# Kernel tuning notes

Measured on AMD Instinct MI355X. Metric: run time of the kernel, lower is better.

The kernel has to match this reference:

```python
import jax, jax.numpy as jnp
import numpy as np

QMIN, QMAX = 0.0, 255.0  # uint8 activation quantization range


def _qlinear(x, w_q, b, s_in, zp_in, s_w):
    """zentorch_qlinear: quantize fp32 x to uint8, int8 weight, dequant output.

    x:   [M, K] fp32
    w_q: [N, K] int8 values (stored int32), symmetric (weight zp = 0)
    b:   [N] fp32
    s_in, zp_in: scalars (activation scale / zero point)
    s_w: [N] per-output-channel weight scales
    """
    zp = zp_in.astype(jnp.float32)
    q = jnp.clip(jnp.round(x / s_in) + zp, QMIN, QMAX)      # fake-quant uint8
    x_dq = (q - zp) * s_in                                   # dequantized activation
    w_dq = w_q.astype(jnp.float32) * s_w[:, None]            # [N, K] dequant weight
    return x_dq @ w_dq.T + b                                 # [M, N] fp32


def setup_inputs() -> dict:
    key = jax.random.key(0)
    k1, k2, k3, k4 = jax.random.split(key, 4)
    M, K, N = 8192, 4096, 4096
    inp = {
        "input": jax.random.normal(k1, (M, K), dtype=jnp.float32),
        "weights": jax.random.randint(k2, (N, K), -128, 128, dtype=jnp.int32),
        "biases": jax.random.normal(k3, (N,), dtype=jnp.float32) * 0.1,
        "input_scales": jnp.array([0.05], dtype=jnp.float32),
        "input_zero_points": jnp.array([128], dtype=jnp.int32),
        "weight_scales": jax.random.uniform(k4, (N,), dtype=jnp.float32, minval=0.001, maxval=0.01),
        "weight_zero_points": jnp.zeros((N,), dtype=jnp.int32),
        "output_dtype": 0,  # 0 -> float32
    }
    return inp


def reference(input, weights, biases, input_scales, input_zero_points,
              weight_scales, weight_zero_points, output_dtype):
    s_in = input_scales[0]
    zp_in = input_zero_points[0]
    x = _qlinear(input, weights, biases, s_in, zp_in, weight_scales)
    x = _qlinear(x, weights, biases, s_in, zp_in, weight_scales)
    x = _qlinear(x, weights, biases, s_in, zp_in, weight_scales)
    return x
```

## Files before the change

kernel.cpp:

```cpp
#include <hip/hip_runtime.h>
#include <stdint.h>

#define M_DIM 8192
#define K_DIM 4096
#define N_DIM 4096
#define KTILES (K_DIM / 64)

typedef __attribute__((ext_vector_type(4))) int i32x4;

__global__ void pack_w_kernel(const int* __restrict__ w, char* __restrict__ wp,
                              int* __restrict__ corr, const int* __restrict__ zpp) {
  __shared__ int red[256];
  const int n = blockIdx.x;
  const int t = threadIdx.x;
  const int4* row = (const int4*)(w + (size_t)n * K_DIM);
  int s = 0;
  int words[4];
#pragma unroll
  for (int u = 0; u < 4; ++u) {
    int4 v = row[t * 4 + u];
    s += v.x + v.y + v.z + v.w;
    words[u] = (v.x & 255) | ((v.y & 255) << 8) | ((v.z & 255) << 16) | (v.w << 24);
  }
  ((int4*)(wp + (size_t)n * K_DIM))[t] = make_int4(words[0], words[1], words[2], words[3]);
  red[t] = s;
  __syncthreads();
  for (int off = 128; off > 0; off >>= 1) {
    if (t < off) red[t] += red[t + off];
    __syncthreads();
  }
  if (t == 0) corr[n] = (128 - zpp[0]) * red[0];
}

__global__ void quant_in_kernel(const float* __restrict__ x, char* __restrict__ q,
                                const float* __restrict__ sp, const int* __restrict__ zpp) {
  const int i = blockIdx.x * blockDim.x + threadIdx.x;
  const float s = sp[0];
  const float zp = (float)zpp[0];
  float4 v = ((const float4*)x)[i];
  float t0 = fminf(fmaxf(rintf(v.x / s) + zp, 0.f), 255.f);
  float t1 = fminf(fmaxf(rintf(v.y / s) + zp, 0.f), 255.f);
  float t2 = fminf(fmaxf(rintf(v.z / s) + zp, 0.f), 255.f);
  float t3 = fminf(fmaxf(rintf(v.w / s) + zp, 0.f), 255.f);
  int b0 = (int)t0 - 128, b1 = (int)t1 - 128, b2 = (int)t2 - 128, b3 = (int)t3 - 128;
  ((int*)q)[i] = (b0 & 255) | ((b1 & 255) << 8) | ((b2 & 255) << 16) | (b3 << 24);
}

#define STAGE16(SRC, DST)                                                     \
  __builtin_amdgcn_global_load_lds(                                           \
      (const __attribute__((address_space(1))) void*)(SRC),                   \
      (__attribute__((address_space(3))) void*)(DST), 16, 0, 0)

#define RD(p) (*(const i32x4*)(p))

#define TILE(SLOT, KSTG, DO_NEXT)                                             \
  {                                                                           \
    const char* bufA_ = &lds[SLOT][0][0];                                     \
    char* nA_ = &lds[((SLOT) + 3) & 3][0][0];                                 \
    char* nB_ = &lds[((SLOT) + 3) & 3][1][0];                                 \
    i32x4 a1_[4];                                                             \
    _Pragma("unroll") for (int i_ = 0; i_ < 4; ++i_)                          \
        a1_[i_] = RD(bufA_ + aoff[4 + i_]);                                   \
    STAGE16(asrc0 + (size_t)(KSTG) * 64, nA_ + o0_);                          \
    STAGE16(asrc1 + (size_t)(KSTG) * 64, nA_ + o1_);                          \
    __builtin_amdgcn_s_setprio(1);                                            \
    _Pragma("unroll") for (int i_ = 0; i_ < 4; ++i_)                          \
        _Pragma("unroll") for (int j_ = 0; j_ < 4; ++j_)                      \
            acc[i_][j_] = __builtin_amdgcn_mfma_i32_16x16x64_i8(              \
                a0[i_], b0[j_], acc[i_][j_], 0, 0, 0);                        \
    __builtin_amdgcn_s_setprio(0);                                            \
    i32x4 ta_[4], tb_[4];                                                     \
    if (DO_NEXT) {                                                            \
      const char* xA_ = &lds[((SLOT) + 1) & 3][0][0];                         \
      const char* xB_ = &lds[((SLOT) + 1) & 3][1][0];                         \
      _Pragma("unroll") for (int i_ = 0; i_ < 4; ++i_)                        \
          ta_[i_] = RD(xA_ + aoff[i_]);                                       \
      _Pragma("unroll") for (int j_ = 0; j_ < 4; ++j_)                        \
          tb_[j_] = RD(xB_ + boff[j_]);                                       \
    }                                                                         \
    STAGE16(bsrc0 + (size_t)(KSTG) * 64, nB_ + o0_);                          \
    STAGE16(bsrc1 + (size_t)(KSTG) * 64, nB_ + o1_);                          \
    __builtin_amdgcn_s_setprio(1);                                            \
    _Pragma("unroll") for (int i_ = 0; i_ < 4; ++i_)                          \
        _Pragma("unroll") for (int j_ = 0; j_ < 4; ++j_)                      \
            acc[4 + i_][j_] = __builtin_amdgcn_mfma_i32_16x16x64_i8(          \
                a1_[i_], b0[j_], acc[4 + i_][j_], 0, 0, 0);                   \
    __builtin_amdgcn_s_setprio(0);                                            \
    asm volatile("s_waitcnt vmcnt(4)" ::: "memory");                          \
    __builtin_amdgcn_s_barrier();                                             \
    if (DO_NEXT) {                                                            \
      _Pragma("unroll") for (int i_ = 0; i_ < 4; ++i_) a0[i_] = ta_[i_];      \
      _Pragma("unroll") for (int j_ = 0; j_ < 4; ++j_) b0[j_] = tb_[j_];      \
    }                                                                         \
  }

template <int WRITE_Q>
__global__ __launch_bounds__(512, 2) void gemm_kernel(
    const char* __restrict__ qa, const char* __restrict__ wb,
    const int* __restrict__ corr, const float* __restrict__ swp,
    const float* __restrict__ bias, const float* __restrict__ sp,
    const int* __restrict__ zpp, char* __restrict__ outq, float* __restrict__ outf) {
  __shared__ __align__(16) char lds[4][2][16384];
  const int tid = threadIdx.x;
  const int lane = tid & 63;
  const int w = tid >> 6;
  const int wr = w >> 2;
  const int wc = w & 3;
  const int bid = blockIdx.x;
  const int bm = bid & 31;
  const int bn = bid >> 5;
  const char* abase = qa + (size_t)bm * 256 * K_DIM;
  const char* bbase = wb + (size_t)bn * 256 * K_DIM;

  const int o0_ = tid * 16;
  const int o1_ = 8192 + tid * 16;
  const int r0_ = o0_ >> 6, r1_ = o1_ >> 6;
  const int g0_ = ((o0_ >> 4) & 3) ^ ((r0_ >> 1) & 3);
  const int g1_ = ((o1_ >> 4) & 3) ^ ((r1_ >> 1) & 3);
  const char* asrc0 = abase + (size_t)r0_ * K_DIM + g0_ * 16;
  const char* asrc1 = abase + (size_t)r1_ * K_DIM + g1_ * 16;
  const char* bsrc0 = bbase + (size_t)r0_ * K_DIM + g0_ * 16;
  const char* bsrc1 = bbase + (size_t)r1_ * K_DIM + g1_ * 16;

  const int rr = lane & 15;
  const int g = lane >> 4;
  int aoff[8], boff[4];
#pragma unroll
  for (int i = 0; i < 8; ++i) {
    const int row = wr * 128 + i * 16 + rr;
    aoff[i] = (row << 6) + ((g ^ ((row >> 1) & 3)) << 4);
  }
#pragma unroll
  for (int j = 0; j < 4; ++j) {
    const int row = wc * 64 + j * 16 + rr;
    boff[j] = (row << 6) + ((g ^ ((row >> 1) & 3)) << 4);
  }

  i32x4 acc[8][4] = {};

  STAGE16(asrc0, &lds[0][0][o0_]); STAGE16(asrc1, &lds[0][0][o1_]);
  STAGE16(bsrc0, &lds[0][1][o0_]); STAGE16(bsrc1, &lds[0][1][o1_]);
  STAGE16(asrc0 + 64, &lds[1][0][o0_]); STAGE16(asrc1 + 64, &lds[1][0][o1_]);
  STAGE16(bsrc0 + 64, &lds[1][1][o0_]); STAGE16(bsrc1 + 64, &lds[1][1][o1_]);
  STAGE16(asrc0 + 128, &lds[2][0][o0_]); STAGE16(asrc1 + 128, &lds[2][0][o1_]);
  STAGE16(bsrc0 + 128, &lds[2][1][o0_]); STAGE16(bsrc1 + 128, &lds[2][1][o1_]);
  asm volatile("s_waitcnt vmcnt(4)" ::: "memory");
  __builtin_amdgcn_s_barrier();

  i32x4 a0[4], b0[4];
#pragma unroll
  for (int i = 0; i < 4; ++i) a0[i] = RD(&lds[0][0][0] + aoff[i]);
#pragma unroll
  for (int j = 0; j < 4; ++j) b0[j] = RD(&lds[0][1][0] + boff[j]);

  for (int tb = 0; tb < (KTILES - 4) / 4; ++tb) {
    const int t0 = tb * 4;
#pragma unroll
    for (int u = 0; u < 4; ++u) {
      TILE(u, t0 + u + 3, 1);
    }
  }
  TILE(0, KTILES - 1, 1);
  TILE(1, KTILES - 1, 1);
  TILE(2, KTILES - 1, 1);
  TILE(3, KTILES - 1, 0);
  asm volatile("s_waitcnt vmcnt(0)" ::: "memory");

  const float s = sp[0];
  const float zpf = (float)zpp[0];
  const int m0 = bm * 256 + wr * 128 + (lane >> 4) * 4;
  const int n0 = bn * 256 + wc * 64 + (lane & 15);
#pragma unroll
  for (int j = 0; j < 4; ++j) {
    const int n = n0 + j * 16;
    const int cr = corr[n];
    const float fs = s * swp[n];
    const float bb = bias[n];
#pragma unroll
    for (int i = 0; i < 8; ++i) {
#pragma unroll
      for (int q = 0; q < 4; ++q) {
        const int m = m0 + i * 16 + q;
        float val = fs * (float)(acc[i][j][q] + cr) + bb;
        if (WRITE_Q) {
          float tq = fminf(fmaxf(rintf(val / s) + zpf, 0.f), 255.f);
          outq[(size_t)m * N_DIM + n] = (char)((int)tq - 128);
        } else {
          outf[(size_t)m * N_DIM + n] = val;
        }
      }
    }
  }
}

extern "C" void kernel_launch(void* const* d_in, const int* in_sizes, int n_in,
                              void* d_out, int out_size, void* d_ws, size_t ws_size,
                              hipStream_t stream) {
  const float* x = (const float*)d_in[0];
  const int* wq = (const int*)d_in[1];
  const float* bias = (const float*)d_in[2];
  const float* s_in = (const float*)d_in[3];
  const int* zp_in = (const int*)d_in[4];
  const float* s_w = (const float*)d_in[5];
  float* out = (float*)d_out;

  const size_t WP_BYTES = (size_t)N_DIM * K_DIM;
  const size_t Q_BYTES = (size_t)M_DIM * K_DIM;
  char* ws = (char*)d_ws;
  char* wp = ws;
  char* q1 = ws + WP_BYTES;
  char* q2 = q1 + Q_BYTES;
  int* corr = (int*)(q2 + Q_BYTES);
  const size_t NEEDED = WP_BYTES + 2 * Q_BYTES + (size_t)N_DIM * sizeof(int);
  if (ws_size < NEEDED) return;

  pack_w_kernel<<<N_DIM, 256, 0, stream>>>(wq, wp, corr, zp_in);
  quant_in_kernel<<<(M_DIM * K_DIM / 4) / 256, 256, 0, stream>>>(x, q1, s_in, zp_in);

  dim3 grid((M_DIM / 256) * (N_DIM / 256));
  dim3 blk(512);
  gemm_kernel<1><<<grid, blk, 0, stream>>>(q1, wp, corr, s_w, bias, s_in, zp_in, q2, nullptr);
  gemm_kernel<1><<<grid, blk, 0, stream>>>(q2, wp, corr, s_w, bias, s_in, zp_in, q1, nullptr);
  gemm_kernel<0><<<grid, blk, 0, stream>>>(q1, wp, corr, s_w, bias, s_in, zp_in, nullptr, out);
}
```

Before: 451.7 us.

## Restructure GEMM main loop into four barrier-interleaved MFMA phases with vectorized epilogue

```diff
diff --git a/kernel.cpp b/kernel.cpp
--- a/kernel.cpp
+++ b/kernel.cpp
@@ -53,45 +53,56 @@
 
 #define RD(p) (*(const i32x4*)(p))
 
-#define TILE(SLOT, KSTG, DO_NEXT)                                             \
+#define BAR __builtin_amdgcn_s_barrier()
+#define LGKM0 asm volatile("s_waitcnt lgkmcnt(0)" ::: "memory")
+#define SCHED0 __builtin_amdgcn_sched_barrier(0)
+
+#define MF8(I0, AV, J0, BV)                                                   \
+  _Pragma("unroll") for (int i_ = 0; i_ < 4; ++i_)                            \
+      _Pragma("unroll") for (int j_ = 0; j_ < 2; ++j_)                        \
+          acc[(I0) + i_][(J0) + j_] = __builtin_amdgcn_mfma_i32_16x16x64_i8(  \
+              AV[i_], BV[j_], acc[(I0) + i_][(J0) + j_], 0, 0, 0);
+
+#define TILE8(SLOT, KSTG)                                                     \
   {                                                                           \
-    const char* bufA_ = &lds[SLOT][0][0];                                     \
+    const char* sA_ = &lds[SLOT][0][0];                                       \
+    const char* sB_ = &lds[SLOT][1][0];                                       \
     char* nA_ = &lds[((SLOT) + 3) & 3][0][0];                                 \
     char* nB_ = &lds[((SLOT) + 3) & 3][1][0];                                 \
-    i32x4 a1_[4];                                                             \
+    i32x4 aL[4], aH[4], bL[2], bH[2];                                         \
+                                             \
     _Pragma("unroll") for (int i_ = 0; i_ < 4; ++i_)                          \
-        a1_[i_] = RD(bufA_ + aoff[4 + i_]);                                   \
-    STAGE16(asrc0 + (size_t)(KSTG) * 64, nA_ + o0_);                          \
-    STAGE16(asrc1 + (size_t)(KSTG) * 64, nA_ + o1_);                          \
-    __builtin_amdgcn_s_setprio(1);                                            \
+        aL[i_] = RD(sA_ + aoff[i_]);                                          \
+    bL[0] = RD(sB_ + boff[0]);                                                \
+    bL[1] = RD(sB_ + boff[1]);                                                \
+    STAGE16(asrc0 + (size_t)(KSTG), nA_ + o0_);                               \
+    BAR; LGKM0; SCHED0;                                                       \
+    __builtin_amdgcn_s_setprio(1); MF8(0, aL, 0, bL)                          \
+    __builtin_amdgcn_s_setprio(0);                                            \
+    BAR;                                                                      \
+                                             \
+    bH[0] = RD(sB_ + boff[2]);                                                \
+    bH[1] = RD(sB_ + boff[3]);                                                \
+    STAGE16(asrc1 + (size_t)(KSTG), nA_ + o1_);                               \
+    BAR; LGKM0; SCHED0;                                                       \
+    __builtin_amdgcn_s_setprio(1); MF8(0, aL, 2, bH)                          \
+    __builtin_amdgcn_s_setprio(0);                                            \
+    BAR;                                                                      \
+                                             \
     _Pragma("unroll") for (int i_ = 0; i_ < 4; ++i_)                          \
-        _Pragma("unroll") for (int j_ = 0; j_ < 4; ++j_)                      \
-            acc[i_][j_] = __builtin_amdgcn_mfma_i32_16x16x64_i8(              \
-                a0[i_], b0[j_], acc[i_][j_], 0, 0, 0);                        \
-    __builtin_amdgcn_s_setprio(0);                                            \
-    i32x4 ta_[4], tb_[4];                                                     \
-    if (DO_NEXT) {                                                            \
-      const char* xA_ = &lds[((SLOT) + 1) & 3][0][0];                         \
-      const char* xB_ = &lds[((SLOT) + 1) & 3][1][0];                         \
-      _Pragma("unroll") for (int i_ = 0; i_ < 4; ++i_)                        \
-          ta_[i_] = RD(xA_ + aoff[i_]);                                       \
-      _Pragma("unroll") for (int j_ = 0; j_ < 4; ++j_)                        \
-          tb_[j_] = RD(xB_ + boff[j_]);                                       \
-    }                                                                         \
-    STAGE16(bsrc0 + (size_t)(KSTG) * 64, nB_ + o0_);                          \
-    STAGE16(bsrc1 + (size_t)(KSTG) * 64, nB_ + o1_);                          \
-    __builtin_amdgcn_s_setprio(1);                                            \
-    _Pragma("unroll") for (int i_ = 0; i_ < 4; ++i_)                          \
-        _Pragma("unroll") for (int j_ = 0; j_ < 4; ++j_)                      \
-            acc[4 + i_][j_] = __builtin_amdgcn_mfma_i32_16x16x64_i8(          \
-                a1_[i_], b0[j_], acc[4 + i_][j_], 0, 0, 0);                   \
-    __builtin_amdgcn_s_setprio(0);                                            \
-    asm volatile("s_waitcnt vmcnt(4)" ::: "memory");                          \
-    __builtin_amdgcn_s_barrier();                                             \
-    if (DO_NEXT) {                                                            \
-      _Pragma("unroll") for (int i_ = 0; i_ < 4; ++i_) a0[i_] = ta_[i_];      \
-      _Pragma("unroll") for (int j_ = 0; j_ < 4; ++j_) b0[j_] = tb_[j_];      \
-    }                                                                         \
+        aH[i_] = RD(sA_ + aoff[4 + i_]);                                      \
+    STAGE16(bsrc0 + (size_t)(KSTG), nB_ + o0_);                               \
+    BAR; LGKM0; SCHED0;                                                       \
+    __builtin_amdgcn_s_setprio(1); MF8(4, aH, 2, bH)                          \
+    __builtin_amdgcn_s_setprio(0);                                            \
+    BAR;                                                                      \
+                                  \
+    STAGE16(bsrc1 + (size_t)(KSTG), nB_ + o1_);                               \
+    BAR; SCHED0;                                                              \
+    __builtin_amdgcn_s_setprio(1); MF8(4, aH, 0, bL)                          \
+    __builtin_amdgcn_s_setprio(0);                                            \
+    asm volatile("s_waitcnt vmcnt(8)" ::: "memory");                          \
+    BAR;                                                                      \
   }
 
 template <int WRITE_Q>
@@ -119,8 +130,10 @@
   const int g1_ = ((o1_ >> 4) & 3) ^ ((r1_ >> 1) & 3);
   const char* asrc0 = abase + (size_t)r0_ * K_DIM + g0_ * 16;
   const char* asrc1 = abase + (size_t)r1_ * K_DIM + g1_ * 16;
-  const char* bsrc0 = bbase + (size_t)r0_ * K_DIM + g0_ * 16;
-  const char* bsrc1 = bbase + (size_t)r1_ * K_DIM + g1_ * 16;
+  const int p0_ = (r0_ & ~63) + 4 * (r0_ & 15) + ((r0_ >> 4) & 3);
+  const int p1_ = (r1_ & ~63) + 4 * (r1_ & 15) + ((r1_ >> 4) & 3);
+  const char* bsrc0 = bbase + (size_t)p0_ * K_DIM + g0_ * 16;
+  const char* bsrc1 = bbase + (size_t)p1_ * K_DIM + g1_ * 16;
 
   const int rr = lane & 15;
   const int g = lane >> 4;
@@ -144,50 +157,48 @@
   STAGE16(bsrc0 + 64, &lds[1][1][o0_]); STAGE16(bsrc1 + 64, &lds[1][1][o1_]);
   STAGE16(asrc0 + 128, &lds[2][0][o0_]); STAGE16(asrc1 + 128, &lds[2][0][o1_]);
   STAGE16(bsrc0 + 128, &lds[2][1][o0_]); STAGE16(bsrc1 + 128, &lds[2][1][o1_]);
-  asm volatile("s_waitcnt vmcnt(4)" ::: "memory");
+  asm volatile("s_waitcnt vmcnt(8)" ::: "memory");
   __builtin_amdgcn_s_barrier();
 
-  i32x4 a0[4], b0[4];
-#pragma unroll
-  for (int i = 0; i < 4; ++i) a0[i] = RD(&lds[0][0][0] + aoff[i]);
-#pragma unroll
-  for (int j = 0; j < 4; ++j) b0[j] = RD(&lds[0][1][0] + boff[j]);
-
-  for (int tb = 0; tb < (KTILES - 4) / 4; ++tb) {
-    const int t0 = tb * 4;
+  for (int tb = 0; tb < KTILES / 4; ++tb) {
 #pragma unroll
     for (int u = 0; u < 4; ++u) {
-      TILE(u, t0 + u + 3, 1);
+      const int t = tb * 4 + u;
+      const int ks_ = (t + 3 < KTILES ? t + 3 : KTILES - 1) * 64;
+      TILE8(u, ks_);
     }
   }
-  TILE(0, KTILES - 1, 1);
-  TILE(1, KTILES - 1, 1);
-  TILE(2, KTILES - 1, 1);
-  TILE(3, KTILES - 1, 0);
   asm volatile("s_waitcnt vmcnt(0)" ::: "memory");
 
   const float s = sp[0];
   const float zpf = (float)zpp[0];
   const int m0 = bm * 256 + wr * 128 + (lane >> 4) * 4;
-  const int n0 = bn * 256 + wc * 64 + (lane & 15);
-#pragma unroll
-  for (int j = 0; j < 4; ++j) {
-    const int n = n0 + j * 16;
-    const int cr = corr[n];
-    const float fs = s * swp[n];
-    const float bb = bias[n];
-#pragma unroll
-    for (int i = 0; i < 8; ++i) {
-#pragma unroll
-      for (int q = 0; q < 4; ++q) {
-        const int m = m0 + i * 16 + q;
-        float val = fs * (float)(acc[i][j][q] + cr) + bb;
-        if (WRITE_Q) {
-          float tq = fminf(fmaxf(rintf(val / s) + zpf, 0.f), 255.f);
-          outq[(size_t)m * N_DIM + n] = (char)((int)tq - 128);
-        } else {
-          outf[(size_t)m * N_DIM + n] = val;
-        }
+  const int nb4 = bn * 256 + wc * 64 + ((lane & 15) << 2);
+  const int4 cr4 = *(const int4*)(corr + nb4);
+  const float4 sw4 = *(const float4*)(swp + nb4);
+  const float4 bb4 = *(const float4*)(bias + nb4);
+  const float fs0 = s * sw4.x, fs1 = s * sw4.y, fs2 = s * sw4.z, fs3 = s * sw4.w;
+#pragma unroll
+  for (int i = 0; i < 8; ++i) {
+#pragma unroll
+    for (int q = 0; q < 4; ++q) {
+      const int m = m0 + i * 16 + q;
+      const float v0 = fs0 * (float)(acc[i][0][q] + cr4.x) + bb4.x;
+      const float v1 = fs1 * (float)(acc[i][1][q] + cr4.y) + bb4.y;
+      const float v2 = fs2 * (float)(acc[i][2][q] + cr4.z) + bb4.z;
+      const float v3 = fs3 * (float)(acc[i][3][q] + cr4.w) + bb4.w;
+      if (WRITE_Q) {
+        const int b0i = (int)fminf(fmaxf(rintf(v0 / s) + zpf, 0.f), 255.f) - 128;
+        const int b1i = (int)fminf(fmaxf(rintf(v1 / s) + zpf, 0.f), 255.f) - 128;
+        const int b2i = (int)fminf(fmaxf(rintf(v2 / s) + zpf, 0.f), 255.f) - 128;
+        const int b3i = (int)fminf(fmaxf(rintf(v3 / s) + zpf, 0.f), 255.f) - 128;
+        const uint32_t pk = (uint32_t)(b0i & 255) | ((uint32_t)(b1i & 255) << 8) |
+                            ((uint32_t)(b2i & 255) << 16) | ((uint32_t)b3i << 24);
+        *(uint32_t*)(outq + (size_t)m * N_DIM + nb4) = pk;
+      } else {
+        float4 o4;
+        o4.x = v0; o4.y = v1; o4.z = v2; o4.w = v3;
+        *(float4*)(outf + (size_t)m * N_DIM + nb4) = o4;
       }
     }
   }
```

Measured after the change: 442.0 us. -2.1%, faster.
